# Performance work log

Measured on AMD Instinct MI355X. Metric: run time of the kernel, lower is better.

## Reference

```python
import jax, jax.numpy as jnp
import numpy as np

N = 131072
DIMS_IN = 16
DIMS_C = 16
UNITS = 512
BINS = 10
MIN_W = 1e-3   # min_bin_width
MIN_H = 1e-3   # min_bin_height
MIN_D = 1e-3   # min_bin_derivative
N_PERMS = 4                 # ceil(log2(DIMS_IN))
BLOCKS = 2 * N_PERMS        # log permutation strategy doubles each bit-mask
DT = DIMS_IN // 2           # transformed dims per block (power-of-2 => exact half)
FEAT_IN = DT + DIMS_C       # subnet input features
FEAT_OUT = DT * (3 * BINS + 1)  # widths+heights+derivatives per transformed dim


def _masks():
    # Reproduces the 'log' permutation mask construction from Flow.__init__
    cm = np.array([[int(b) for b in np.binary_repr(j, N_PERMS)] for j in range(DIMS_IN)])
    cm = cm[:, ::-1].astype(bool).T           # (N_PERMS, DIMS_IN)
    m = np.repeat(cm, 2, axis=0)              # (BLOCKS, DIMS_IN)
    m[1::2] = ~m[1::2]
    return m  # True = condition dim, False = transformed dim


def _mlp(h, W0, b0, W1, b1, W2, b2):
    # layers=3 -> Linear/ReLU/Linear/ReLU/Linear
    h = jax.nn.relu(h @ W0 + b0)
    h = jax.nn.relu(h @ W1 + b1)
    return h @ W2 + b2


def _rqs_forward(x, uw, uh, ud):
    # x: (n, DT) in [0,1]; uw/uh: (n, DT, BINS); ud: (n, DT, BINS+1)
    w = MIN_W + (1.0 - MIN_W * BINS) * jax.nn.softmax(uw, axis=-1)
    h = MIN_H + (1.0 - MIN_H * BINS) * jax.nn.softmax(uh, axis=-1)
    d = MIN_D + jax.nn.softplus(ud)
    zero = jnp.zeros(w.shape[:-1] + (1,), w.dtype)
    cw = jnp.concatenate([zero, jnp.cumsum(w, axis=-1)], axis=-1)  # knot x-positions
    ch = jnp.concatenate([zero, jnp.cumsum(h, axis=-1)], axis=-1)  # knot y-positions
    # bin search: index of bin containing x
    idx = jnp.clip(jnp.sum(x[..., None] >= cw, axis=-1) - 1, 0, BINS - 1)
    take = lambda a, i: jnp.take_along_axis(a, i[..., None], axis=-1)[..., 0]
    xk, wk = take(cw, idx), take(w, idx)
    yk, hk = take(ch, idx), take(h, idx)
    dk, dk1 = take(d, idx), take(d, idx + 1)
    theta = jnp.clip((x - xk) / wk, 0.0, 1.0)
    s = hk / wk
    t1 = theta * (1.0 - theta)
    denom = s + (dk1 + dk - 2.0 * s) * t1
    y = yk + hk * (s * theta * theta + dk * t1) / denom
    logdet = (2.0 * jnp.log(s)
              + jnp.log(dk1 * theta * theta + 2.0 * s * t1 + dk * (1.0 - theta) ** 2)
              - 2.0 * jnp.log(denom))
    return y, logdet


def _log_prob(x, c, W0, b0, W1, b1, W2, b2):
    masks = _masks()
    z = x
    logdet = jnp.zeros(x.shape[0], x.dtype)
    for b in range(BLOCKS):
        m = masks[b]
        cond_idx = np.where(m)[0]
        trans_idx = np.where(~m)[0]
        subnet_in = jnp.concatenate([z[:, cond_idx], c], axis=-1)  # (n, FEAT_IN)
        params = _mlp(subnet_in, W0[b], b0[b], W1[b], b1[b], W2[b], b2[b])
        params = params.reshape(-1, DT, 3 * BINS + 1)
        uw, uh, ud = params[..., :BINS], params[..., BINS:2 * BINS], params[..., 2 * BINS:]
        y, lj = _rqs_forward(z[:, trans_idx], uw, uh, ud)
        logdet = logdet + jnp.sum(lj, axis=-1)
        z = z.at[:, trans_idx].set(y)
    # uniform latent on [0,1]^d => latent log-density is 0
    return logdet


def setup_inputs() -> dict:
    key = jax.random.key(0)
    ks = jax.random.split(key, 6)
    x = jax.random.uniform(ks[0], (N, DIMS_IN), jnp.float32)
    c = jax.random.normal(ks[1], (N, DIMS_C), jnp.float32)
    W0 = jax.random.normal(ks[2], (BLOCKS, FEAT_IN, UNITS), jnp.float32) / np.sqrt(FEAT_IN)
    W1 = jax.random.normal(ks[3], (BLOCKS, UNITS, UNITS), jnp.float32) / np.sqrt(UNITS)
    W2 = jax.random.normal(ks[4], (BLOCKS, UNITS, FEAT_OUT), jnp.float32) / np.sqrt(UNITS)
    b0 = jnp.zeros((BLOCKS, UNITS), jnp.float32)
    b1 = jnp.zeros((BLOCKS, UNITS), jnp.float32)
    b2 = jnp.zeros((BLOCKS, FEAT_OUT), jnp.float32)
    return {"x": x, "c": c, "W0": W0, "b0": b0, "W1": W1, "b1": b1, "W2": W2, "b2": b2}


def reference(x, c, W0, b0, W1, b1, W2, b2):
    return _log_prob(x, c, W0, b0, W1, b1, W2, b2)
```

## Files before the change

### kernel.cpp

```cpp
#include <hip/hip_runtime.h>
#include <math.h>

#define NROWS 131072
#define DIN   16
#define DC    16
#define UNITS 512
#define BINS  10
#define DT    8
#define FOUT  248
#define M_TILE 64
#define NWG   (NROWS / M_TILE)

#define Z_OFF    0u
#define W0F_OFF  8388608u
#define W1F_OFF  8650752u
#define W2F_OFF  12845056u

typedef _Float16 h16x8 __attribute__((ext_vector_type(8)));
typedef float    f32x4 __attribute__((ext_vector_type(4)));

union Frag { h16x8 v; uint4 q; unsigned int u32[4]; _Float16 h[8]; };

static __device__ inline unsigned int pack2h(float lo, float hi) {
    union { _Float16 h[2]; unsigned int u; } x;
    x.h[0] = (_Float16)lo; x.h[1] = (_Float16)hi;
    return x.u;
}

static __device__ inline float fast_rcp(float x) { return __builtin_amdgcn_rcpf(x); }

__global__ __launch_bounds__(256)
void prep_weights(const float* __restrict__ W0, const float* __restrict__ W1,
                  const float* __restrict__ W2, _Float16* __restrict__ W0F,
                  _Float16* __restrict__ W1F, _Float16* __restrict__ W2F)
{
    const int idx = blockIdx.x * 256 + threadIdx.x;
    const int SZ0 = 8 * 32 * 512;
    const int SZ1 = 8 * 32 * 16 * 512;
    const int SZ2 = 8 * 16 * 4 * 4 * 512;
    if (idx < SZ0) {
        int b = idx >> 14, r = idx & 16383;
        int ut = r >> 9, le = r & 511;
        int lane = le >> 3, j = le & 7;
        int quad = lane >> 4, l15 = lane & 15;
        int m = ut * 16 + l15, k = quad * 8 + j;
        W0F[idx] = (k < 24) ? (_Float16)W0[b * (24 * 512) + k * 512 + m] : (_Float16)0.f;
    } else if (idx < SZ0 + SZ1) {
        int i = idx - SZ0;
        int b = i >> 18, r = i & 262143;
        int ut = r >> 13, r2 = r & 8191;
        int ks = r2 >> 9, le = r2 & 511;
        int lane = le >> 3, j = le & 7;
        int quad = lane >> 4, l15 = lane & 15;
        int m = ut * 16 + l15, k = ks * 32 + quad * 8 + j;
        W1F[i] = (_Float16)W1[(b << 18) + k * 512 + m];
    } else if (idx < SZ0 + SZ1 + SZ2) {
        int i = idx - SZ0 - SZ1;
        int b = i >> 17, r = i & 131071;
        int ut2 = r >> 13, r2 = r & 8191;
        int c2 = r2 >> 11, r3 = r2 & 2047;
        int ks2 = r3 >> 9, le = r3 & 511;
        int lane = le >> 3, j = le & 7;
        int quad = lane >> 4, l15 = lane & 15;
        int m = ut2 * 16 + l15, k = c2 * 128 + ks2 * 32 + quad * 8 + j;
        W2F[i] = (m < FOUT) ? (_Float16)W2[b * (512 * FOUT) + k * FOUT + m] : (_Float16)0.f;
    }
}

__global__ __launch_bounds__(512, 4)
void flow_block_kernel(const float* __restrict__ z, const float* __restrict__ c,
                       const _Float16* __restrict__ W0F, const float* __restrict__ b0,
                       const _Float16* __restrict__ W1F, const float* __restrict__ b1,
                       const _Float16* __restrict__ W2F, const float* __restrict__ b2,
                       float* __restrict__ zout, float* __restrict__ logdet,
                       int p, int inv)
{
    __shared__ __align__(16) char smem[65536];

    const int t    = threadIdx.x;
    const int wave = t >> 6;
    const int lane = t & 63;
    const int quad = lane >> 4;
    const int l15  = lane & 15;
    const int row0 = blockIdx.x * M_TILE;
    const int lowmask = (1 << p) - 1;
    const int cv = 1 - inv, tv = inv;
    const int lofs = lane * 8;

    Frag bx[4];
    #pragma unroll
    for (int rt = 0; rt < 4; ++rt) {
        const int n = rt * 16 + l15;
        const float* zr = z + (size_t)(row0 + n) * DIN;
        const float* cr = c + (size_t)(row0 + n) * DC;
        float v[8];
        if (quad == 0) {
            #pragma unroll
            for (int j = 0; j < 8; ++j) {
                const int col = ((j >> p) << (p + 1)) | (cv << p) | (j & lowmask);
                v[j] = zr[col];
            }
        } else if (quad == 1) {
            #pragma unroll
            for (int j = 0; j < 8; ++j) v[j] = cr[j];
        } else if (quad == 2) {
            #pragma unroll
            for (int j = 0; j < 8; ++j) v[j] = cr[8 + j];
        } else {
            #pragma unroll
            for (int j = 0; j < 8; ++j) v[j] = 0.f;
        }
        #pragma unroll
        for (int j = 0; j < 4; ++j) bx[rt].u32[j] = pack2h(v[2 * j], v[2 * j + 1]);
    }

    #pragma unroll
    for (int j = 0; j < 4; ++j) {
        const int ut = wave * 4 + j;
        Frag a; a.q = *(const uint4*)(W0F + (ut << 9) + lofs);
        const f32x4 bias = *(const f32x4*)(b0 + ut * 16 + quad * 4);
        const int m0 = ut * 16 + quad * 4;
        #pragma unroll
        for (int rt = 0; rt < 4; ++rt) {
            f32x4 acc = __builtin_amdgcn_mfma_f32_16x16x32_f16(a.v, bx[rt].v, bias, 0, 0, 0);
            const int n = rt * 16 + l15;
            uint2 w2;
            w2.x = pack2h(fmaxf(acc.x, 0.f), fmaxf(acc.y, 0.f));
            w2.y = pack2h(fmaxf(acc.z, 0.f), fmaxf(acc.w, 0.f));
            const int addr = n * 1024 + (((m0 >> 3) ^ (n & 7)) * 16) + ((m0 & 4) * 2);
            *(uint2*)(smem + addr) = w2;
        }
    }
    __syncthreads();

    f32x4 h1[4][4];
    #pragma unroll
    for (int j = 0; j < 4; ++j) {
        const int ut = wave * 4 + j;
        const f32x4 bias = *(const f32x4*)(b1 + ut * 16 + quad * 4);
        #pragma unroll
        for (int rt = 0; rt < 4; ++rt) h1[j][rt] = bias;
    }
    #pragma unroll 4
    for (int ks = 0; ks < 16; ++ks) {
        Frag B[4];
        #pragma unroll
        for (int rt = 0; rt < 4; ++rt) {
            const int n = rt * 16 + l15;
            B[rt].v = *(const h16x8*)(smem + n * 1024 + (((ks * 4 + quad) ^ (n & 7)) * 16));
        }
        __builtin_amdgcn_s_setprio(1);
        #pragma unroll
        for (int j = 0; j < 4; ++j) {
            const int ut = wave * 4 + j;
            Frag a; a.q = *(const uint4*)(W1F + (((ut << 4) + ks) << 9) + lofs);
            #pragma unroll
            for (int rt = 0; rt < 4; ++rt)
                h1[j][rt] = __builtin_amdgcn_mfma_f32_16x16x32_f16(a.v, B[rt].v, h1[j][rt], 0, 0, 0);
        }
        __builtin_amdgcn_s_setprio(0);
    }
    __syncthreads();

    #pragma unroll
    for (int j = 0; j < 4; ++j) {
        const int ut = wave * 4 + j;
        const int m0 = ut * 16 + quad * 4;
        #pragma unroll
        for (int rt = 0; rt < 4; ++rt) {
            const int n = rt * 16 + l15;
            uint2 w2;
            w2.x = pack2h(fmaxf(h1[j][rt].x, 0.f), fmaxf(h1[j][rt].y, 0.f));
            w2.y = pack2h(fmaxf(h1[j][rt].z, 0.f), fmaxf(h1[j][rt].w, 0.f));
            const int addr = n * 1024 + (((m0 >> 3) ^ (n & 7)) * 16) + ((m0 & 4) * 2);
            *(uint2*)(smem + addr) = w2;
        }
    }
    __syncthreads();

    f32x4 pacc[2][4];
    #pragma unroll
    for (int i2 = 0; i2 < 2; ++i2) {
        const int m0 = (wave * 2 + i2) * 16 + quad * 4;
        f32x4 bias;
        if (m0 < FOUT) bias = *(const f32x4*)(b2 + m0);
        else { bias.x = 0.f; bias.y = 0.f; bias.z = 0.f; bias.w = 0.f; }
        #pragma unroll
        for (int rt = 0; rt < 4; ++rt) pacc[i2][rt] = bias;
    }
    #pragma unroll 4
    for (int kk = 0; kk < 16; ++kk) {
        const int kc = kk * 4 + quad;
        Frag B[4];
        #pragma unroll
        for (int rt = 0; rt < 4; ++rt) {
            const int n = rt * 16 + l15;
            B[rt].v = *(const h16x8*)(smem + n * 1024 + ((kc ^ (n & 7)) * 16));
        }
        __builtin_amdgcn_s_setprio(1);
        #pragma unroll
        for (int i2 = 0; i2 < 2; ++i2) {
            const int ut2 = wave * 2 + i2;
            Frag a; a.q = *(const uint4*)(W2F + (((ut2 << 4) + kk) << 9) + lofs);
            #pragma unroll
            for (int rt = 0; rt < 4; ++rt)
                pacc[i2][rt] = __builtin_amdgcn_mfma_f32_16x16x32_f16(a.v, B[rt].v, pacc[i2][rt], 0, 0, 0);
        }
        __builtin_amdgcn_s_setprio(0);
    }
    __syncthreads();

    #pragma unroll
    for (int i2 = 0; i2 < 2; ++i2) {
        const int m0 = (wave * 2 + i2) * 16 + quad * 4;
        if (m0 < FOUT) {
            #pragma unroll
            for (int rt = 0; rt < 4; ++rt) {
                const int n = rt * 16 + l15;
                *(f32x4*)(smem + n * 1008 + m0 * 4) = pacc[i2][rt];
            }
        }
    }
    __syncthreads();

    {
        const int r = t >> 3;
        const int d = t & 7;
        const int row = row0 + r;
        const int td = ((d >> p) << (p + 1)) | (tv << p) | (d & lowmask);

        const float x = z[(size_t)row * DIN + td];

        const float* pp = (const float*)(smem + r * 1008) + d * 31;
        float pv[31];
        #pragma unroll
        for (int i = 0; i < 31; ++i) pv[i] = pp[i];

        float mw = pv[0];
        #pragma unroll
        for (int i = 1; i < BINS; ++i) mw = fmaxf(mw, pv[i]);
        float w[BINS]; float sw = 0.f;
        #pragma unroll
        for (int i = 0; i < BINS; ++i) { w[i] = __expf(pv[i] - mw); sw += w[i]; }
        const float rw = (1.0f - 0.001f * BINS) * fast_rcp(sw);
        #pragma unroll
        for (int i = 0; i < BINS; ++i) w[i] = 0.001f + rw * w[i];

        float mh = pv[BINS];
        #pragma unroll
        for (int i = 1; i < BINS; ++i) mh = fmaxf(mh, pv[BINS + i]);
        float hh[BINS]; float sh = 0.f;
        #pragma unroll
        for (int i = 0; i < BINS; ++i) { hh[i] = __expf(pv[BINS + i] - mh); sh += hh[i]; }
        const float rh = (1.0f - 0.001f * BINS) * fast_rcp(sh);
        #pragma unroll
        for (int i = 0; i < BINS; ++i) hh[i] = 0.001f + rh * hh[i];

        float cw[BINS], ch[BINS];
        cw[0] = 0.f; ch[0] = 0.f;
        #pragma unroll
        for (int i = 0; i < BINS - 1; ++i) { cw[i + 1] = cw[i] + w[i]; ch[i + 1] = ch[i] + hh[i]; }

        float xk = cw[0], wk = w[0], yk = ch[0], hk = hh[0];
        float uk = pv[2 * BINS], uk1 = pv[2 * BINS + 1];
        #pragma unroll
        for (int i = 1; i < BINS; ++i) {
            const bool sel = (x >= cw[i]);
            xk  = sel ? cw[i]            : xk;
            wk  = sel ? w[i]             : wk;
            yk  = sel ? ch[i]            : yk;
            hk  = sel ? hh[i]            : hk;
            uk  = sel ? pv[2 * BINS + i]     : uk;
            uk1 = sel ? pv[2 * BINS + i + 1] : uk1;
        }
        const float dk  = 0.001f + fmaxf(uk, 0.f)  + __logf(1.f + __expf(-fabsf(uk)));
        const float dk1 = 0.001f + fmaxf(uk1, 0.f) + __logf(1.f + __expf(-fabsf(uk1)));

        const float inv_wk = fast_rcp(wk);
        float th = (x - xk) * inv_wk;
        th = fminf(fmaxf(th, 0.f), 1.f);
        const float s   = hk * inv_wk;
        const float t1  = th * (1.f - th);
        const float den = s + (dk1 + dk - 2.f * s) * t1;
        const float inv_den = fast_rcp(den);
        const float num = s * th * th + dk * t1;
        const float y   = yk + hk * num * inv_den;
        const float om  = 1.f - th;
        const float r1  = s * inv_den;
        const float q   = r1 * r1 * (dk1 * th * th + 2.f * s * t1 + dk * om * om);
        float ljv = __logf(q);

        zout[(size_t)row * DIN + td] = y;

        float v = ljv;
        v += __shfl_down(v, 4, 8);
        v += __shfl_down(v, 2, 8);
        v += __shfl_down(v, 1, 8);
        if ((t & 7) == 0) logdet[row0 + (t >> 3)] += v;
    }
}

extern "C" void kernel_launch(void* const* d_in, const int* in_sizes, int n_in,
                              void* d_out, int out_size, void* d_ws, size_t ws_size,
                              hipStream_t stream) {
    (void)in_sizes; (void)n_in; (void)out_size; (void)ws_size;
    const float* x  = (const float*)d_in[0];
    const float* c  = (const float*)d_in[1];
    const float* W0 = (const float*)d_in[2];
    const float* b0 = (const float*)d_in[3];
    const float* W1 = (const float*)d_in[4];
    const float* b1 = (const float*)d_in[5];
    const float* W2 = (const float*)d_in[6];
    const float* b2 = (const float*)d_in[7];
    float* out = (float*)d_out;

    char* ws = (char*)d_ws;
    float* z = (float*)(ws + Z_OFF);
    _Float16* W0F = (_Float16*)(ws + W0F_OFF);
    _Float16* W1F = (_Float16*)(ws + W1F_OFF);
    _Float16* W2F = (_Float16*)(ws + W2F_OFF);

    hipMemcpyAsync(z, x, (size_t)NROWS * DIN * sizeof(float),
                   hipMemcpyDeviceToDevice, stream);
    hipMemsetAsync(out, 0, (size_t)NROWS * sizeof(float), stream);

    prep_weights<<<12800, 256, 0, stream>>>(W0, W1, W2, W0F, W1F, W2F);

    dim3 grid(NWG), block(512);
    for (int b = 0; b < 8; ++b) {
        const int p = b >> 1, inv = b & 1;
        flow_block_kernel<<<grid, block, 0, stream>>>(
            z, c,
            W0F + (size_t)b * 32 * 512,          b0 + (size_t)b * UNITS,
            W1F + (size_t)b * 32 * 16 * 512,     b1 + (size_t)b * UNITS,
            W2F + (size_t)b * 16 * 4 * 4 * 512,  b2 + (size_t)b * FOUT,
            z, out, p, inv);
    }
}
```

Measured before the change: 1.013 ms.

## Switch hidden and output GEMMs to 32x32x16 MFMA with repacked weights

Replaces the 16x16x32 MFMA tiles in the second and third MLP layers with 32x32x16 f16 MFMA. The weight prepacking is reorganised to match the new fragment layout, and the LDS fragment loads and result write-backs are remapped to match. The larger tiles are meant to cut LDS B-fragment reads and A-fragment global loads per flop, and to use the higher-throughput instruction shape. In exchange, each wave holds 16-wide accumulator vectors, which may raise register pressure.

```diff
diff --git a/kernel.cpp b/kernel.cpp
--- a/kernel.cpp
+++ b/kernel.cpp
@@ -18,6 +18,7 @@
 
 typedef _Float16 h16x8 __attribute__((ext_vector_type(8)));
 typedef float    f32x4 __attribute__((ext_vector_type(4)));
+typedef float    f32x16 __attribute__((ext_vector_type(16)));
 
 union Frag { h16x8 v; uint4 q; unsigned int u32[4]; _Float16 h[8]; };
 
@@ -36,8 +37,8 @@
 {
     const int idx = blockIdx.x * 256 + threadIdx.x;
     const int SZ0 = 8 * 32 * 512;
-    const int SZ1 = 8 * 32 * 16 * 512;
-    const int SZ2 = 8 * 16 * 4 * 4 * 512;
+    const int SZ1 = 8 * 16 * 32 * 512;
+    const int SZ2 = 8 * 8 * 32 * 512;
     if (idx < SZ0) {
         int b = idx >> 14, r = idx & 16383;
         int ut = r >> 9, le = r & 511;
@@ -48,22 +49,21 @@
     } else if (idx < SZ0 + SZ1) {
         int i = idx - SZ0;
         int b = i >> 18, r = i & 262143;
-        int ut = r >> 13, r2 = r & 8191;
+        int ut32 = r >> 14, r2 = r & 16383;
         int ks = r2 >> 9, le = r2 & 511;
         int lane = le >> 3, j = le & 7;
-        int quad = lane >> 4, l15 = lane & 15;
-        int m = ut * 16 + l15, k = ks * 32 + quad * 8 + j;
+        int m = ut32 * 32 + (lane & 31);
+        int k = ks * 16 + (lane >> 5) * 8 + j;
         W1F[i] = (_Float16)W1[(b << 18) + k * 512 + m];
     } else if (idx < SZ0 + SZ1 + SZ2) {
         int i = idx - SZ0 - SZ1;
         int b = i >> 17, r = i & 131071;
-        int ut2 = r >> 13, r2 = r & 8191;
-        int c2 = r2 >> 11, r3 = r2 & 2047;
-        int ks2 = r3 >> 9, le = r3 & 511;
+        int ut232 = r >> 14, r2 = r & 16383;
+        int kk = r2 >> 9, le = r2 & 511;
         int lane = le >> 3, j = le & 7;
-        int quad = lane >> 4, l15 = lane & 15;
-        int m = ut2 * 16 + l15, k = c2 * 128 + ks2 * 32 + quad * 8 + j;
-        W2F[i] = (m < FOUT) ? (_Float16)W2[b * (512 * FOUT) + k * FOUT + m] : (_Float16)0.f;
+        int m2 = ut232 * 32 + (lane & 31);
+        int k = kk * 16 + (lane >> 5) * 8 + j;
+        W2F[i] = (m2 < FOUT) ? (_Float16)W2[b * (512 * FOUT) + k * FOUT + m2] : (_Float16)0.f;
     }
 }
 
@@ -82,6 +82,8 @@
     const int lane = t & 63;
     const int quad = lane >> 4;
     const int l15  = lane & 15;
+    const int l31  = lane & 31;
+    const int half = lane >> 5;
     const int row0 = blockIdx.x * M_TILE;
     const int lowmask = (1 << p) - 1;
     const int cv = 1 - inv, tv = inv;
@@ -133,91 +135,101 @@
     }
     __syncthreads();
 
-    f32x4 h1[4][4];
-    #pragma unroll
-    for (int j = 0; j < 4; ++j) {
-        const int ut = wave * 4 + j;
-        const f32x4 bias = *(const f32x4*)(b1 + ut * 16 + quad * 4);
-        #pragma unroll
-        for (int rt = 0; rt < 4; ++rt) h1[j][rt] = bias;
+    f32x16 h1a[2][2];
+    #pragma unroll
+    for (int i = 0; i < 2; ++i) {
+        const int base = (wave * 2 + i) * 32;
+        #pragma unroll
+        for (int g = 0; g < 4; ++g) {
+            const f32x4 bb = *(const f32x4*)(b1 + base + 8 * g + 4 * half);
+            #pragma unroll
+            for (int rt = 0; rt < 2; ++rt) {
+                h1a[i][rt][4 * g + 0] = bb.x; h1a[i][rt][4 * g + 1] = bb.y;
+                h1a[i][rt][4 * g + 2] = bb.z; h1a[i][rt][4 * g + 3] = bb.w;
+            }
+        }
     }
     #pragma unroll 4
-    for (int ks = 0; ks < 16; ++ks) {
-        Frag B[4];
-        #pragma unroll
-        for (int rt = 0; rt < 4; ++rt) {
-            const int n = rt * 16 + l15;
-            B[rt].v = *(const h16x8*)(smem + n * 1024 + (((ks * 4 + quad) ^ (n & 7)) * 16));
+    for (int ks = 0; ks < 32; ++ks) {
+        Frag B[2];
+        #pragma unroll
+        for (int rt = 0; rt < 2; ++rt) {
+            const int n = rt * 32 + l31;
+            B[rt].v = *(const h16x8*)(smem + n * 1024 + (((ks * 2 + half) ^ (n & 7)) * 16));
         }
         __builtin_amdgcn_s_setprio(1);
         #pragma unroll
-        for (int j = 0; j < 4; ++j) {
-            const int ut = wave * 4 + j;
-            Frag a; a.q = *(const uint4*)(W1F + (((ut << 4) + ks) << 9) + lofs);
-            #pragma unroll
-            for (int rt = 0; rt < 4; ++rt)
-                h1[j][rt] = __builtin_amdgcn_mfma_f32_16x16x32_f16(a.v, B[rt].v, h1[j][rt], 0, 0, 0);
+        for (int i = 0; i < 2; ++i) {
+            Frag a; a.q = *(const uint4*)(W1F + ((((wave * 2 + i) * 32) + ks) << 9) + lofs);
+            #pragma unroll
+            for (int rt = 0; rt < 2; ++rt)
+                h1a[i][rt] = __builtin_amdgcn_mfma_f32_32x32x16_f16(a.v, B[rt].v, h1a[i][rt], 0, 0, 0);
         }
         __builtin_amdgcn_s_setprio(0);
     }
     __syncthreads();
 
     #pragma unroll
-    for (int j = 0; j < 4; ++j) {
-        const int ut = wave * 4 + j;
-        const int m0 = ut * 16 + quad * 4;
-        #pragma unroll
-        for (int rt = 0; rt < 4; ++rt) {
-            const int n = rt * 16 + l15;
-            uint2 w2;
-            w2.x = pack2h(fmaxf(h1[j][rt].x, 0.f), fmaxf(h1[j][rt].y, 0.f));
-            w2.y = pack2h(fmaxf(h1[j][rt].z, 0.f), fmaxf(h1[j][rt].w, 0.f));
-            const int addr = n * 1024 + (((m0 >> 3) ^ (n & 7)) * 16) + ((m0 & 4) * 2);
-            *(uint2*)(smem + addr) = w2;
-        }
-    }
-    __syncthreads();
-
-    f32x4 pacc[2][4];
-    #pragma unroll
-    for (int i2 = 0; i2 < 2; ++i2) {
-        const int m0 = (wave * 2 + i2) * 16 + quad * 4;
-        f32x4 bias;
-        if (m0 < FOUT) bias = *(const f32x4*)(b2 + m0);
-        else { bias.x = 0.f; bias.y = 0.f; bias.z = 0.f; bias.w = 0.f; }
-        #pragma unroll
-        for (int rt = 0; rt < 4; ++rt) pacc[i2][rt] = bias;
+    for (int i = 0; i < 2; ++i) {
+        #pragma unroll
+        for (int rt = 0; rt < 2; ++rt) {
+            const int n = rt * 32 + l31;
+            #pragma unroll
+            for (int g = 0; g < 4; ++g) {
+                const int m = (wave * 2 + i) * 32 + 8 * g + 4 * half;
+                uint2 w2;
+                w2.x = pack2h(fmaxf(h1a[i][rt][4 * g + 0], 0.f), fmaxf(h1a[i][rt][4 * g + 1], 0.f));
+                w2.y = pack2h(fmaxf(h1a[i][rt][4 * g + 2], 0.f), fmaxf(h1a[i][rt][4 * g + 3], 0.f));
+                const int addr = n * 1024 + (((m >> 3) ^ (n & 7)) * 16) + ((m & 4) * 2);
+                *(uint2*)(smem + addr) = w2;
+            }
+        }
+    }
+    __syncthreads();
+
+    f32x16 pa[2];
+    #pragma unroll
+    for (int g = 0; g < 4; ++g) {
+        const int m2 = wave * 32 + 8 * g + 4 * half;
+        f32x4 bb;
+        if (m2 < FOUT) bb = *(const f32x4*)(b2 + m2);
+        else { bb.x = 0.f; bb.y = 0.f; bb.z = 0.f; bb.w = 0.f; }
+        #pragma unroll
+        for (int rt = 0; rt < 2; ++rt) {
+            pa[rt][4 * g + 0] = bb.x; pa[rt][4 * g + 1] = bb.y;
+            pa[rt][4 * g + 2] = bb.z; pa[rt][4 * g + 3] = bb.w;
+        }
     }
     #pragma unroll 4
-    for (int kk = 0; kk < 16; ++kk) {
-        const int kc = kk * 4 + quad;
-        Frag B[4];
-        #pragma unroll
-        for (int rt = 0; rt < 4; ++rt) {
-            const int n = rt * 16 + l15;
-            B[rt].v = *(const h16x8*)(smem + n * 1024 + ((kc ^ (n & 7)) * 16));
+    for (int kk = 0; kk < 32; ++kk) {
+        Frag B[2];
+        #pragma unroll
+        for (int rt = 0; rt < 2; ++rt) {
+            const int n = rt * 32 + l31;
+            B[rt].v = *(const h16x8*)(smem + n * 1024 + (((kk * 2 + half) ^ (n & 7)) * 16));
         }
         __builtin_amdgcn_s_setprio(1);
-        #pragma unroll
-        for (int i2 = 0; i2 < 2; ++i2) {
-            const int ut2 = wave * 2 + i2;
-            Frag a; a.q = *(const uint4*)(W2F + (((ut2 << 4) + kk) << 9) + lofs);
-            #pragma unroll
-            for (int rt = 0; rt < 4; ++rt)
-                pacc[i2][rt] = __builtin_amdgcn_mfma_f32_16x16x32_f16(a.v, B[rt].v, pacc[i2][rt], 0, 0, 0);
+        {
+            Frag a; a.q = *(const uint4*)(W2F + (((wave * 32) + kk) << 9) + lofs);
+            #pragma unroll
+            for (int rt = 0; rt < 2; ++rt)
+                pa[rt] = __builtin_amdgcn_mfma_f32_32x32x16_f16(a.v, B[rt].v, pa[rt], 0, 0, 0);
         }
         __builtin_amdgcn_s_setprio(0);
     }
     __syncthreads();
 
     #pragma unroll
-    for (int i2 = 0; i2 < 2; ++i2) {
-        const int m0 = (wave * 2 + i2) * 16 + quad * 4;
-        if (m0 < FOUT) {
-            #pragma unroll
-            for (int rt = 0; rt < 4; ++rt) {
-                const int n = rt * 16 + l15;
-                *(f32x4*)(smem + n * 1008 + m0 * 4) = pacc[i2][rt];
+    for (int rt = 0; rt < 2; ++rt) {
+        const int n = rt * 32 + l31;
+        #pragma unroll
+        for (int g = 0; g < 4; ++g) {
+            const int m2 = wave * 32 + 8 * g + 4 * half;
+            if (m2 < FOUT) {
+                f32x4 o;
+                o.x = pa[rt][4 * g + 0]; o.y = pa[rt][4 * g + 1];
+                o.z = pa[rt][4 * g + 2]; o.w = pa[rt][4 * g + 3];
+                *(f32x4*)(smem + n * 1008 + m2 * 4) = o;
             }
         }
     }
@@ -332,8 +344,8 @@
         flow_block_kernel<<<grid, block, 0, stream>>>(
             z, c,
             W0F + (size_t)b * 32 * 512,          b0 + (size_t)b * UNITS,
-            W1F + (size_t)b * 32 * 16 * 512,     b1 + (size_t)b * UNITS,
-            W2F + (size_t)b * 16 * 4 * 4 * 512,  b2 + (size_t)b * FOUT,
+            W1F + (size_t)b * 16 * 32 * 512,     b1 + (size_t)b * UNITS,
+            W2F + (size_t)b * 8 * 32 * 512,      b2 + (size_t)b * FOUT,
             z, out, p, inv);
     }
 }
```

Result: slower. 1.143 ms (+12.9%).
